# Kernel tuning notes

Measured on AMD Instinct MI355X. Metric: run time of the kernel, lower is better.

## Reference

```python
import jax, jax.numpy as jnp
import numpy as np

T, B, D = 32, 16, 128


def _evolve(xr, xi, U):
    # xr, xi: [T,B,D,D]; U: [D,D,2] -> complex U x U^H per matrix
    Ur, Ui = U[..., 0], U[..., 1]
    r = jnp.einsum('ij,tbjk->tbik', Ur, xr) - jnp.einsum('ij,tbjk->tbik', Ui, xi)
    i = jnp.einsum('ij,tbjk->tbik', Ui, xr) + jnp.einsum('ij,tbjk->tbik', Ur, xi)
    out_r = jnp.einsum('tbik,jk->tbij', r, Ur) + jnp.einsum('tbik,jk->tbij', i, Ui)
    out_i = jnp.einsum('tbik,jk->tbij', i, Ur) - jnp.einsum('tbik,jk->tbij', r, Ui)
    return out_r, out_i


def _forward(inputs_real, inputs_imag, Uq, Uk, Uv):
    qr, qi = _evolve(inputs_real, inputs_imag, Uq)
    kr, ki = _evolve(inputs_real, inputs_imag, Uk)
    vr, vi = _evolve(inputs_real, inputs_imag, Uv)
    # trace(A @ B) = sum_ij A_ij * B_ji -> distance scores [Tq, Tk, B]
    tr_r = jnp.einsum('qbij,kbji->qkb', qr, kr) - jnp.einsum('qbij,kbji->qkb', qi, ki)
    tr_i = jnp.einsum('qbij,kbji->qkb', qr, ki) + jnp.einsum('qbij,kbji->qkb', qi, kr)
    dist = jnp.sqrt(tr_r * tr_r + tr_i * tr_i)
    # original builds scores via torch.tensor(list) -> values are detached
    dist = jax.lax.stop_gradient(dist)
    # original applies softmax over the LAST dim of the [Tk, B] score matrix,
    # i.e. over the batch dim (faithful reproduction)
    S = jax.nn.softmax(dist, axis=-1)  # [Tq, Tk, B]
    # original zip(values[0], values[1], scores) iterates the (real, imag)
    # components of the value at t=0 and t=1 against score rows 0 and 1
    s0 = S[:, 0, :, None, None]  # [Tq,B,1,1]
    s1 = S[:, 1, :, None, None]
    out_r = vr[0][None] * s0 + vi[0][None] * s1  # [Tq,B,D,D]
    out_i = vr[1][None] * s0 + vi[1][None] * s1
    return out_r, out_i


def setup_inputs() -> dict:
    key = jax.random.key(0)
    k0, k1, k2, k3, k4 = jax.random.split(key, 5)
    inputs_real = jax.random.normal(k0, (T, B, D, D), dtype=jnp.float32)
    inputs_imag = jax.random.normal(k1, (T, B, D, D), dtype=jnp.float32)
    eye = jnp.stack([jnp.eye(D, dtype=jnp.float32), jnp.zeros((D, D), jnp.float32)], axis=-1)
    Uq = eye + 0.05 * jax.random.normal(k2, (D, D, 2), dtype=jnp.float32)
    Uk = eye + 0.05 * jax.random.normal(k3, (D, D, 2), dtype=jnp.float32)
    Uv = eye + 0.05 * jax.random.normal(k4, (D, D, 2), dtype=jnp.float32)
    return {"inputs_real": inputs_real, "inputs_imag": inputs_imag, "Uq": Uq, "Uk": Uk, "Uv": Uv}


def reference(inputs_real, inputs_imag, Uq, Uk, Uv):
    return _forward(inputs_real, inputs_imag, Uq, Uk, Uv)
```

## Files before the change

### kernel.cpp

```cpp
#include <hip/hip_runtime.h>
#include <math.h>

#define MAT 16384
#define OFF_MR   0
#define OFF_MI   16384
#define OFF_MTR  32768
#define OFF_MTI  49152
#define OFF_UVTR 65536
#define OFF_UVTI 81920
#define OFF_ZSR  2129920
#define OFF_ZSI  (OFF_ZSR + 32*16384)
#define OFF_VR   (OFF_ZSI + 32*16384)
#define OFF_VI   (OFF_VR + 32*16384)
#define OFF_TR   (OFF_VI + 32*16384)
#define OFF_S    (OFF_TR + 2048)

__device__ __forceinline__ float dot4(float4 a, float4 b) {
    return a.x*b.x + a.y*b.y + a.z*b.z + a.w*b.w;
}

__global__ __launch_bounds__(128) void k_M(const float* __restrict__ Uq,
                                           const float* __restrict__ Uk,
                                           const float* __restrict__ Uv,
                                           float* __restrict__ ws) {
    const int i = blockIdx.x;
    const int j = threadIdx.x;
    __shared__ float qr_s[128], qi_s[128];
    qr_s[j] = Uq[(j*128 + i)*2 + 0];
    qi_s[j] = Uq[(j*128 + i)*2 + 1];
    __syncthreads();
    const float2* Uk2 = (const float2*)Uk;
    float mr = 0.f, mi = 0.f;
    #pragma unroll 8
    for (int p = 0; p < 128; ++p) {
        float2 k2 = Uk2[p*128 + j];
        float qr = qr_s[p], qi = qi_s[p];
        mr += qr*k2.x + qi*k2.y;
        mi += qr*k2.y - qi*k2.x;
    }
    ws[OFF_MR  + i*128 + j] = mr;
    ws[OFF_MI  + i*128 + j] = mi;
    ws[OFF_MTR + j*128 + i] = mr;
    ws[OFF_MTI + j*128 + i] = mi;
    float2 uv = ((const float2*)Uv)[i*128 + j];
    ws[OFF_UVTR + j*128 + i] = uv.x;
    ws[OFF_UVTI + j*128 + i] = uv.y;
}

__global__ __launch_bounds__(256) void k_fused(const float* __restrict__ xr,
                                               const float* __restrict__ xi,
                                               const float* __restrict__ Uv,
                                               float* __restrict__ ws) {
    const int bid = blockIdx.x;
    const int m   = bid & 63;
    const int i0  = (bid >> 6) * 8;
    const int tid = threadIdx.x;
    const int rp  = tid & 3;
    const int cg  = tid >> 2;

    __shared__ __align__(16) float smem_f[2048 + 4096];
    float* At   = smem_f;
    float* Bbuf = smem_f + 2048;

    float accr[2][2], acci[2][2];
    #pragma unroll
    for (int r = 0; r < 2; ++r)
        #pragma unroll
        for (int k = 0; k < 2; ++k) { accr[r][k] = 0.f; acci[r][k] = 0.f; }

    const float2* Uv2 = (const float2*)Uv;
    const float4* Xr4 = (const float4*)(xr + (m & 31)*MAT);
    const float4* Xi4 = (const float4*)(xi + (m & 31)*MAT);
    const float4* P2r = (const float4*)(ws + (m < 32 ? OFF_MTR : OFF_UVTR));
    const float4* P2i = (const float4*)(ws + (m < 32 ? OFF_MTI : OFF_UVTI));

    #pragma unroll
    for (int w = 0; w < 2; ++w) {
        int slot = w*256 + tid;
        int rs = slot & 3;
        int p  = slot >> 2;
        float ar0, ai0, ar1, ai1;
        if (m < 32) {
            ar0 = ws[OFF_MR + (i0 + rs*2    )*128 + p];
            ai0 = ws[OFF_MI + (i0 + rs*2    )*128 + p];
            ar1 = ws[OFF_MR + (i0 + rs*2 + 1)*128 + p];
            ai1 = ws[OFF_MI + (i0 + rs*2 + 1)*128 + p];
        } else {
            float2 u0 = Uv2[(i0 + rs*2    )*128 + p];
            float2 u1 = Uv2[(i0 + rs*2 + 1)*128 + p];
            ar0 = u0.x; ai0 = u0.y; ar1 = u1.x; ai1 = u1.y;
        }
        *(float4*)&At[p*16 + rs*4] = make_float4(ar0, ai0, ar1, ai1);
    }

    float4 pr0, pr1, pi0, pi1;
    auto gload = [&](const float4* R, const float4* I, int t) {
        int b0 = t*512;
        pr0 = R[b0 + tid];
        pr1 = R[b0 + 256 + tid];
        pi0 = I[b0 + tid];
        pi1 = I[b0 + 256 + tid];
    };
    auto writeB = [&]() {
        ((float4*)Bbuf)[tid]                = pr0;
        ((float4*)Bbuf)[tid + 256]          = pr1;
        ((float4*)(Bbuf + 2048))[tid]       = pi0;
        ((float4*)(Bbuf + 2048))[tid + 256] = pi1;
    };

    gload(Xr4, Xi4, 0); writeB(); __syncthreads();
    for (int t = 0; t < 8; ++t) {
        if (t < 7) gload(Xr4, Xi4, t+1);
        #pragma unroll
        for (int pp = 0; pp < 16; ++pp) {
            int p = (t<<4) + pp;
            float4 a4  = *(const float4*)&At[p*16 + (rp<<2)];
            float2 brv = *(const float2*)&Bbuf[pp*128 + (cg<<1)];
            float2 biv = *(const float2*)&Bbuf[2048 + pp*128 + (cg<<1)];
            accr[0][0] += a4.x*brv.x - a4.y*biv.x;
            acci[0][0] += a4.x*biv.x + a4.y*brv.x;
            accr[0][1] += a4.x*brv.y - a4.y*biv.y;
            acci[0][1] += a4.x*biv.y + a4.y*brv.y;
            accr[1][0] += a4.z*brv.x - a4.w*biv.x;
            acci[1][0] += a4.z*biv.x + a4.w*brv.x;
            accr[1][1] += a4.z*brv.y - a4.w*biv.y;
            acci[1][1] += a4.z*biv.y + a4.w*brv.y;
        }
        __syncthreads();
        if (t < 7) { writeB(); __syncthreads(); }
    }

    gload(P2r, P2i, 0);
    #pragma unroll
    for (int k = 0; k < 2; ++k)
        *(float4*)&At[((cg<<1)+k)*16 + (rp<<2)] =
            make_float4(accr[0][k], acci[0][k], accr[1][k], acci[1][k]);
    #pragma unroll
    for (int r = 0; r < 2; ++r)
        #pragma unroll
        for (int k = 0; k < 2; ++k) { accr[r][k] = 0.f; acci[r][k] = 0.f; }
    writeB();
    __syncthreads();

    for (int t = 0; t < 8; ++t) {
        if (t < 7) gload(P2r, P2i, t+1);
        #pragma unroll
        for (int k2 = 0; k2 < 16; ++k2) {
            int k = (t<<4) + k2;
            float4 a4  = *(const float4*)&At[k*16 + (rp<<2)];
            float2 urv = *(const float2*)&Bbuf[k2*128 + (cg<<1)];
            float2 uiv = *(const float2*)&Bbuf[2048 + k2*128 + (cg<<1)];
            accr[0][0] += a4.x*urv.x + a4.y*uiv.x;
            acci[0][0] += a4.y*urv.x - a4.x*uiv.x;
            accr[0][1] += a4.x*urv.y + a4.y*uiv.y;
            acci[0][1] += a4.y*urv.y - a4.x*uiv.y;
            accr[1][0] += a4.z*urv.x + a4.w*uiv.x;
            acci[1][0] += a4.w*urv.x - a4.z*uiv.x;
            accr[1][1] += a4.z*urv.y + a4.w*uiv.y;
            acci[1][1] += a4.w*urv.y - a4.z*uiv.y;
        }
        __syncthreads();
        if (t < 7) { writeB(); __syncthreads(); }
    }

    if (m < 32) {
        float* T_r = Bbuf;
        float* T_i = Bbuf + 1056;
        #pragma unroll
        for (int r = 0; r < 2; ++r)
            #pragma unroll
            for (int k = 0; k < 2; ++k) {
                T_r[((rp<<1)+r)*132 + (cg<<1)+k] = accr[r][k];
                T_i[((rp<<1)+r)*132 + (cg<<1)+k] = acci[r][k];
            }
        __syncthreads();
        float* dstR = ws + OFF_ZSR + m*MAT;
        float* dstI = ws + OFF_ZSI + m*MAT;
        #pragma unroll
        for (int w = 0; w < 4; ++w) {
            int o  = w*256 + tid;
            int c  = o >> 3;
            int ii = o & 7;
            dstR[c*128 + i0 + ii] = T_r[ii*132 + c];
            dstI[c*128 + i0 + ii] = T_i[ii*132 + c];
        }
    } else {
        float* dstR = ws + OFF_VR + (m-32)*MAT;
        float* dstI = ws + OFF_VI + (m-32)*MAT;
        #pragma unroll
        for (int r = 0; r < 2; ++r) {
            *(float2*)&dstR[(i0 + (rp<<1) + r)*128 + (cg<<1)] =
                make_float2(accr[r][0], accr[r][1]);
            *(float2*)&dstI[(i0 + (rp<<1) + r)*128 + (cg<<1)] =
                make_float2(acci[r][0], acci[r][1]);
        }
    }
}

__global__ __launch_bounds__(256) void k_trace(const float* __restrict__ xr,
                                               const float* __restrict__ xi,
                                               float* __restrict__ ws) {
    const int q = blockIdx.x >> 4, b = blockIdx.x & 15;
    const int tid = threadIdx.x;
    const float4* Xr4  = (const float4*)(xr + (q*16 + b)*MAT);
    const float4* Xi4  = (const float4*)(xi + (q*16 + b)*MAT);
    const float4* Z0r4 = (const float4*)(ws + OFF_ZSR + b*MAT);
    const float4* Z0i4 = (const float4*)(ws + OFF_ZSI + b*MAT);
    const float4* Z1r4 = (const float4*)(ws + OFF_ZSR + (16+b)*MAT);
    const float4* Z1i4 = (const float4*)(ws + OFF_ZSI + (16+b)*MAT);
    float r0 = 0.f, s0 = 0.f, r1 = 0.f, s1 = 0.f;
    #pragma unroll 4
    for (int w = 0; w < 16; ++w) {
        int e = w*256 + tid;
        float4 xrv = Xr4[e], xiv = Xi4[e];
        float4 z0r = Z0r4[e], z0i = Z0i4[e];
        float4 z1r = Z1r4[e], z1i = Z1i4[e];
        r0 += dot4(xrv, z0r) - dot4(xiv, z0i);
        s0 += dot4(xrv, z0i) + dot4(xiv, z0r);
        r1 += dot4(xrv, z1r) - dot4(xiv, z1i);
        s1 += dot4(xrv, z1i) + dot4(xiv, z1r);
    }
    #pragma unroll
    for (int off = 32; off > 0; off >>= 1) {
        r0 += __shfl_down(r0, off);
        s0 += __shfl_down(s0, off);
        r1 += __shfl_down(r1, off);
        s1 += __shfl_down(s1, off);
    }
    __shared__ float red[4][4];
    if ((tid & 63) == 0) {
        int wv = tid >> 6;
        red[wv][0] = r0; red[wv][1] = s0; red[wv][2] = r1; red[wv][3] = s1;
    }
    __syncthreads();
    if (tid == 0) {
        float a0 = red[0][0]+red[1][0]+red[2][0]+red[3][0];
        float a1 = red[0][1]+red[1][1]+red[2][1]+red[3][1];
        float a2 = red[0][2]+red[1][2]+red[2][2]+red[3][2];
        float a3 = red[0][3]+red[1][3]+red[2][3]+red[3][3];
        float* trp = ws + OFF_TR;
        trp[((q*2+0)*16 + b)*2 + 0] = a0;
        trp[((q*2+0)*16 + b)*2 + 1] = a1;
        trp[((q*2+1)*16 + b)*2 + 0] = a2;
        trp[((q*2+1)*16 + b)*2 + 1] = a3;
    }
}

__global__ __launch_bounds__(64) void k_softmax(float* __restrict__ ws) {
    const int t = threadIdx.x;
    const float* trp = ws + OFF_TR + t*32;
    float d[16];
    float mx = -1e30f;
    #pragma unroll
    for (int b = 0; b < 16; ++b) {
        float rr = trp[b*2+0], ii = trp[b*2+1];
        d[b] = sqrtf(rr*rr + ii*ii);
        mx = fmaxf(mx, d[b]);
    }
    float sum = 0.f;
    #pragma unroll
    for (int b = 0; b < 16; ++b) { d[b] = expf(d[b] - mx); sum += d[b]; }
    float inv = 1.f / sum;
    #pragma unroll
    for (int b = 0; b < 16; ++b) ws[OFF_S + t*16 + b] = d[b] * inv;
}

__global__ __launch_bounds__(256) void k_out(const float* __restrict__ ws,
                                             float* __restrict__ out) {
    const int t = blockIdx.x >> 4, b = blockIdx.x & 15;
    const float s0 = ws[OFF_S + (t*2+0)*16 + b];
    const float s1 = ws[OFF_S + (t*2+1)*16 + b];
    const float4* Vr0 = (const float4*)(ws + OFF_VR + b*MAT);
    const float4* Vi0 = (const float4*)(ws + OFF_VI + b*MAT);
    const float4* Vr1 = (const float4*)(ws + OFF_VR + (16+b)*MAT);
    const float4* Vi1 = (const float4*)(ws + OFF_VI + (16+b)*MAT);
    float4* outR = (float4*)out + (t*16 + b)*4096;
    float4* outI = (float4*)out + 2097152 + (t*16 + b)*4096;
    #pragma unroll 4
    for (int w = 0; w < 16; ++w) {
        int e = w*256 + threadIdx.x;
        float4 a = Vr0[e], bb = Vi0[e], c = Vr1[e], dd = Vi1[e];
        outR[e] = make_float4(a.x*s0 + bb.x*s1, a.y*s0 + bb.y*s1,
                              a.z*s0 + bb.z*s1, a.w*s0 + bb.w*s1);
        outI[e] = make_float4(c.x*s0 + dd.x*s1, c.y*s0 + dd.y*s1,
                              c.z*s0 + dd.z*s1, c.w*s0 + dd.w*s1);
    }
}

extern "C" void kernel_launch(void* const* d_in, const int* in_sizes, int n_in,
                              void* d_out, int out_size, void* d_ws, size_t ws_size,
                              hipStream_t stream) {
    const float* xr = (const float*)d_in[0];
    const float* xi = (const float*)d_in[1];
    const float* Uq = (const float*)d_in[2];
    const float* Uk = (const float*)d_in[3];
    const float* Uv = (const float*)d_in[4];
    float* ws  = (float*)d_ws;
    float* out = (float*)d_out;

    k_M<<<128, 128, 0, stream>>>(Uq, Uk, Uv, ws);
    k_fused<<<1024, 256, 0, stream>>>(xr, xi, Uv, ws);
    k_trace<<<512, 256, 0, stream>>>(xr, xi, ws);
    k_softmax<<<1, 64, 0, stream>>>(ws);
    k_out<<<512, 256, 0, stream>>>(ws, out);
}
```

Before: 99.26 us.

## Give each wavefront private double-buffered LDS column slice to drop block barriers

The fused evolve kernel now gives each of the four wavefronts its own 32-column slice of the B operand in shared memory. Each slice is double-buffered and filled only by that wavefront, so the two block-wide __syncthreads per k-tile in both GEMM phases go away. Global loads are also issued two tiles ahead. This removes barrier stalls and overlaps loads with compute, at the cost of more LDS (40KB vs 24KB), which may lower occupancy, plus a reliance on implicit intra-wavefront ordering of LDS writes and reads.

After: 92.52 us. 6.8% less time.

```diff
diff --git a/kernel.cpp b/kernel.cpp
--- a/kernel.cpp
+++ b/kernel.cpp
@@ -51,16 +51,20 @@
                                                const float* __restrict__ xi,
                                                const float* __restrict__ Uv,
                                                float* __restrict__ ws) {
-    const int bid = blockIdx.x;
-    const int m   = bid & 63;
-    const int i0  = (bid >> 6) * 8;
-    const int tid = threadIdx.x;
-    const int rp  = tid & 3;
-    const int cg  = tid >> 2;
-
-    __shared__ __align__(16) float smem_f[2048 + 4096];
-    float* At   = smem_f;
-    float* Bbuf = smem_f + 2048;
+    const int bid  = blockIdx.x;
+    const int m    = bid & 63;
+    const int i0   = (bid >> 6) * 8;
+    const int tid  = threadIdx.x;
+    const int wv   = tid >> 6;
+    const int lane = tid & 63;
+    const int rp   = lane & 3;
+    const int cp   = lane >> 2;
+    const int j8   = lane & 7;
+    const int rr   = lane >> 3;
+
+    __shared__ __align__(16) float smem[2048 + 4*2048];
+    float* At = smem;
+    float* Sl = smem + 2048 + wv*2048;
 
     float accr[2][2], acci[2][2];
     #pragma unroll
@@ -69,10 +73,10 @@
         for (int k = 0; k < 2; ++k) { accr[r][k] = 0.f; acci[r][k] = 0.f; }
 
     const float2* Uv2 = (const float2*)Uv;
-    const float4* Xr4 = (const float4*)(xr + (m & 31)*MAT);
-    const float4* Xi4 = (const float4*)(xi + (m & 31)*MAT);
-    const float4* P2r = (const float4*)(ws + (m < 32 ? OFF_MTR : OFF_UVTR));
-    const float4* P2i = (const float4*)(ws + (m < 32 ? OFF_MTI : OFF_UVTI));
+    const float4* B1r = (const float4*)(xr + (m & 31)*MAT);
+    const float4* B1i = (const float4*)(xi + (m & 31)*MAT);
+    const float4* B2r = (const float4*)(ws + (m < 32 ? OFF_MTR : OFF_UVTR));
+    const float4* B2i = (const float4*)(ws + (m < 32 ? OFF_MTI : OFF_UVTI));
 
     #pragma unroll
     for (int w = 0; w < 2; ++w) {
@@ -92,86 +96,88 @@
         }
         *(float4*)&At[p*16 + rs*4] = make_float4(ar0, ai0, ar1, ai1);
     }
-
-    float4 pr0, pr1, pi0, pi1;
+    __syncthreads();
+
+    float4 qr0, qr1, qi0, qi1;
     auto gload = [&](const float4* R, const float4* I, int t) {
-        int b0 = t*512;
-        pr0 = R[b0 + tid];
-        pr1 = R[b0 + 256 + tid];
-        pi0 = I[b0 + tid];
-        pi1 = I[b0 + 256 + tid];
+        int base = (t*16 + rr)*32 + wv*8 + j8;
+        qr0 = R[base];       qr1 = R[base + 256];
+        qi0 = I[base];       qi1 = I[base + 256];
     };
-    auto writeB = [&]() {
-        ((float4*)Bbuf)[tid]                = pr0;
-        ((float4*)Bbuf)[tid + 256]          = pr1;
-        ((float4*)(Bbuf + 2048))[tid]       = pi0;
-        ((float4*)(Bbuf + 2048))[tid + 256] = pi1;
+    auto swrite = [&](int h) {
+        float* d = Sl + h*1024;
+        *(float4*)&d[rr*32 + (j8<<2)]           = qr0;
+        *(float4*)&d[(rr+8)*32 + (j8<<2)]       = qr1;
+        *(float4*)&d[512 + rr*32 + (j8<<2)]     = qi0;
+        *(float4*)&d[512 + (rr+8)*32 + (j8<<2)] = qi1;
     };
 
-    gload(Xr4, Xi4, 0); writeB(); __syncthreads();
+    gload(B1r, B1i, 0); swrite(0); gload(B1r, B1i, 1);
     for (int t = 0; t < 8; ++t) {
-        if (t < 7) gload(Xr4, Xi4, t+1);
+        const int h = t & 1;
+        const float* sr = Sl + h*1024;
+        const float* si = sr + 512;
         #pragma unroll
         for (int pp = 0; pp < 16; ++pp) {
-            int p = (t<<4) + pp;
-            float4 a4  = *(const float4*)&At[p*16 + (rp<<2)];
-            float2 brv = *(const float2*)&Bbuf[pp*128 + (cg<<1)];
-            float2 biv = *(const float2*)&Bbuf[2048 + pp*128 + (cg<<1)];
-            accr[0][0] += a4.x*brv.x - a4.y*biv.x;
-            acci[0][0] += a4.x*biv.x + a4.y*brv.x;
-            accr[0][1] += a4.x*brv.y - a4.y*biv.y;
-            acci[0][1] += a4.x*biv.y + a4.y*brv.y;
-            accr[1][0] += a4.z*brv.x - a4.w*biv.x;
-            acci[1][0] += a4.z*biv.x + a4.w*brv.x;
-            accr[1][1] += a4.z*brv.y - a4.w*biv.y;
-            acci[1][1] += a4.z*biv.y + a4.w*brv.y;
-        }
+            float4 a4 = *(const float4*)&At[((t<<4)+pp)*16 + (rp<<2)];
+            float2 br = *(const float2*)&sr[pp*32 + (cp<<1)];
+            float2 bi = *(const float2*)&si[pp*32 + (cp<<1)];
+            accr[0][0] += a4.x*br.x - a4.y*bi.x;
+            acci[0][0] += a4.x*bi.x + a4.y*br.x;
+            accr[0][1] += a4.x*br.y - a4.y*bi.y;
+            acci[0][1] += a4.x*bi.y + a4.y*br.y;
+            accr[1][0] += a4.z*br.x - a4.w*bi.x;
+            acci[1][0] += a4.z*bi.x + a4.w*br.x;
+            accr[1][1] += a4.z*br.y - a4.w*bi.y;
+            acci[1][1] += a4.z*bi.y + a4.w*br.y;
+        }
+        if (t < 7) { swrite((t+1)&1); if (t < 6) gload(B1r, B1i, t+2); }
+    }
+
+    gload(B2r, B2i, 0);
+    __syncthreads();
+    *(float4*)&At[(wv*32 + (cp<<1)    )*16 + (rp<<2)] =
+        make_float4(accr[0][0], acci[0][0], accr[1][0], acci[1][0]);
+    *(float4*)&At[(wv*32 + (cp<<1) + 1)*16 + (rp<<2)] =
+        make_float4(accr[0][1], acci[0][1], accr[1][1], acci[1][1]);
+    #pragma unroll
+    for (int r = 0; r < 2; ++r)
+        #pragma unroll
+        for (int k = 0; k < 2; ++k) { accr[r][k] = 0.f; acci[r][k] = 0.f; }
+    __syncthreads();
+
+    swrite(0); gload(B2r, B2i, 1);
+    for (int t = 0; t < 8; ++t) {
+        const int h = t & 1;
+        const float* sr = Sl + h*1024;
+        const float* si = sr + 512;
+        #pragma unroll
+        for (int k2 = 0; k2 < 16; ++k2) {
+            float4 a4 = *(const float4*)&At[((t<<4)+k2)*16 + (rp<<2)];
+            float2 ur = *(const float2*)&sr[k2*32 + (cp<<1)];
+            float2 ui = *(const float2*)&si[k2*32 + (cp<<1)];
+            accr[0][0] += a4.x*ur.x + a4.y*ui.x;
+            acci[0][0] += a4.y*ur.x - a4.x*ui.x;
+            accr[0][1] += a4.x*ur.y + a4.y*ui.y;
+            acci[0][1] += a4.y*ur.y - a4.x*ui.y;
+            accr[1][0] += a4.z*ur.x + a4.w*ui.x;
+            acci[1][0] += a4.w*ur.x - a4.z*ui.x;
+            accr[1][1] += a4.z*ur.y + a4.w*ui.y;
+            acci[1][1] += a4.w*ur.y - a4.z*ui.y;
+        }
+        if (t < 7) { swrite((t+1)&1); if (t < 6) gload(B2r, B2i, t+2); }
+    }
+
+    if (m < 32) {
         __syncthreads();
-        if (t < 7) { writeB(); __syncthreads(); }
-    }
-
-    gload(P2r, P2i, 0);
-    #pragma unroll
-    for (int k = 0; k < 2; ++k)
-        *(float4*)&At[((cg<<1)+k)*16 + (rp<<2)] =
-            make_float4(accr[0][k], acci[0][k], accr[1][k], acci[1][k]);
-    #pragma unroll
-    for (int r = 0; r < 2; ++r)
-        #pragma unroll
-        for (int k = 0; k < 2; ++k) { accr[r][k] = 0.f; acci[r][k] = 0.f; }
-    writeB();
-    __syncthreads();
-
-    for (int t = 0; t < 8; ++t) {
-        if (t < 7) gload(P2r, P2i, t+1);
-        #pragma unroll
-        for (int k2 = 0; k2 < 16; ++k2) {
-            int k = (t<<4) + k2;
-            float4 a4  = *(const float4*)&At[k*16 + (rp<<2)];
-            float2 urv = *(const float2*)&Bbuf[k2*128 + (cg<<1)];
-            float2 uiv = *(const float2*)&Bbuf[2048 + k2*128 + (cg<<1)];
-            accr[0][0] += a4.x*urv.x + a4.y*uiv.x;
-            acci[0][0] += a4.y*urv.x - a4.x*uiv.x;
-            accr[0][1] += a4.x*urv.y + a4.y*uiv.y;
-            acci[0][1] += a4.y*urv.y - a4.x*uiv.y;
-            accr[1][0] += a4.z*urv.x + a4.w*uiv.x;
-            acci[1][0] += a4.w*urv.x - a4.z*uiv.x;
-            accr[1][1] += a4.z*urv.y + a4.w*uiv.y;
-            acci[1][1] += a4.w*urv.y - a4.z*uiv.y;
-        }
-        __syncthreads();
-        if (t < 7) { writeB(); __syncthreads(); }
-    }
-
-    if (m < 32) {
-        float* T_r = Bbuf;
-        float* T_i = Bbuf + 1056;
+        float* T_r = smem + 2048;
+        float* T_i = smem + 2048 + 1056;
         #pragma unroll
         for (int r = 0; r < 2; ++r)
             #pragma unroll
             for (int k = 0; k < 2; ++k) {
-                T_r[((rp<<1)+r)*132 + (cg<<1)+k] = accr[r][k];
-                T_i[((rp<<1)+r)*132 + (cg<<1)+k] = acci[r][k];
+                T_r[((rp<<1)+r)*132 + wv*32 + (cp<<1)+k] = accr[r][k];
+                T_i[((rp<<1)+r)*132 + wv*32 + (cp<<1)+k] = acci[r][k];
             }
         __syncthreads();
         float* dstR = ws + OFF_ZSR + m*MAT;
@@ -189,9 +195,9 @@
         float* dstI = ws + OFF_VI + (m-32)*MAT;
         #pragma unroll
         for (int r = 0; r < 2; ++r) {
-            *(float2*)&dstR[(i0 + (rp<<1) + r)*128 + (cg<<1)] =
+            *(float2*)&dstR[(i0 + (rp<<1) + r)*128 + wv*32 + (cp<<1)] =
                 make_float2(accr[r][0], accr[r][1]);
-            *(float2*)&dstI[(i0 + (rp<<1) + r)*128 + (cg<<1)] =
+            *(float2*)&dstI[(i0 + (rp<<1) + r)*128 + wv*32 + (cp<<1)] =
                 make_float2(acci[r][0], acci[r][1]);
         }
     }
```
